# Performance work log

Hardware: AMD Instinct MI355X
Metric: run time of the kernel (lower is better)

The kernel has to match this reference:

```python
import jax, jax.numpy as jnp
import numpy as np

B, S, D, H, DK, DV, DFF = 16, 1024, 512, 8, 64, 64, 2048


def _layernorm(x, g, b, eps):
    mu = jnp.mean(x, axis=-1, keepdims=True)
    var = jnp.mean((x - mu) ** 2, axis=-1, keepdims=True)
    return (x - mu) / jnp.sqrt(var + eps) * g + b


def setup_inputs() -> dict:
    key = jax.random.key(0)
    ks = jax.random.split(key, 18)
    def lin_w(k, out_d, in_d):
        lim = np.sqrt(6.0 / (in_d + out_d))  # xavier_uniform
        return jax.random.uniform(k, (out_d, in_d), jnp.float32, -lim, lim)
    return {
        'x': jax.random.normal(ks[0], (B, S, D), jnp.float32),
        'wq': lin_w(ks[1], H * DK, D), 'bq': jnp.zeros((H * DK,), jnp.float32),
        'wk': lin_w(ks[2], H * DK, D), 'bk': jnp.zeros((H * DK,), jnp.float32),
        'wv': lin_w(ks[3], H * DV, D), 'bv': jnp.zeros((H * DV,), jnp.float32),
        'wfc': lin_w(ks[4], D, H * DV), 'bfc': jnp.zeros((D,), jnp.float32),
        'ln1_g': jnp.ones((D,), jnp.float32), 'ln1_b': jnp.zeros((D,), jnp.float32),
        'w1f': lin_w(ks[5], DFF, D), 'b1f': jnp.zeros((DFF,), jnp.float32),
        'w2f': lin_w(ks[6], D, DFF), 'b2f': jnp.zeros((D,), jnp.float32),
        'ln2_g': jnp.ones((D,), jnp.float32), 'ln2_b': jnp.zeros((D,), jnp.float32),
        'current': 1,
    }


def reference(x, wq, bq, wk, bk, wv, bv, wfc, bfc, ln1_g, ln1_b,
              w1f, b1f, w2f, b2f, ln2_g, ln2_b, current):
    b, s, d = x.shape
    # QKV projections -> (b, h, s, d_head)
    q = (x @ wq.T + bq).reshape(b, s, H, DK).transpose(0, 2, 1, 3)
    k = (x @ wk.T + bk).reshape(b, s, H, DK).transpose(0, 2, 1, 3)
    v = (x @ wv.T + bv).reshape(b, s, H, DV).transpose(0, 2, 1, 3)
    # causal mask with variable diagonal (tril(ones, diagonal=-current))
    mask = jnp.tril(jnp.ones((s, s), jnp.float32), k=-int(current))
    temperature = jnp.float32(DK) ** 0.5
    scores = jnp.einsum('bhqd,bhkd->bhqk', q / temperature, k)
    scores = jnp.where(mask == 0, jnp.float32(-1e32), scores)
    attn = jax.nn.softmax(scores, axis=-1)  # [b,h,s,s]
    if int(current) == 1:  # zero-pad first query row
        attn = attn.at[:, :, 0, :].set(0.0)
    attn = attn * mask  # post-softmax mask multiply
    out = jnp.einsum('bhqk,bhkd->bhqd', attn, v)
    out = out.transpose(0, 2, 1, 3).reshape(b, s, H * DV)
    out = out @ wfc.T + bfc + x  # fc + residual (dropout = identity in eval)
    out = _layernorm(out, ln1_g, ln1_b, 1e-5)
    # position-wise FFN
    h = jax.nn.relu(out @ w1f.T + b1f)
    y = h @ w2f.T + b2f + out
    y = _layernorm(y, ln2_g, ln2_b, 1e-6)
    return y
```

## Files before the change

kernel.cpp:

```cpp
#include <hip/hip_runtime.h>
#include <hip/hip_bf16.h>
#include <stdint.h>
#include <stddef.h>

#define NB 16
#define NS 1024
#define ND 512
#define NH 8
#define NDFF 2048
#define NTOK (NB * NS)
#define LDK 1024

typedef __bf16 bf16;
typedef __attribute__((ext_vector_type(2))) __bf16 bf16x2;
typedef __attribute__((ext_vector_type(4))) __bf16 bf16x4;
typedef __attribute__((ext_vector_type(8))) __bf16 bf16x8;
typedef __attribute__((ext_vector_type(4))) float f32x4;

__device__ __forceinline__ void async_copy16(const void* g, void* l) {
  __builtin_amdgcn_global_load_lds(
      (const __attribute__((address_space(1))) void*)g,
      (__attribute__((address_space(3))) void*)l,
      16, 0, 0);
}

__global__ __launch_bounds__(256) void cvt_all(
    const float* __restrict__ x, const float* __restrict__ wq,
    const float* __restrict__ wk, const float* __restrict__ wv,
    const float* __restrict__ wfc, const float* __restrict__ w1f,
    const float* __restrict__ w2f,
    bf16* __restrict__ xb, bf16* __restrict__ w3b,
    bf16* __restrict__ wfcb, bf16* __restrict__ w1fb, bf16* __restrict__ w2fb) {
  constexpr int C0 = 2097152, C1 = C0 + 65536, C2 = C1 + 65536, C3 = C2 + 65536,
                C4 = C3 + 65536, C5 = C4 + 262144;
  const int i = blockIdx.x * 256 + threadIdx.x;
  const float* s;
  bf16* d;
  int base;
  if (i < C0)      { s = x;   d = xb;            base = 0;  }
  else if (i < C1) { s = wq;  d = w3b;           base = C0; }
  else if (i < C2) { s = wk;  d = w3b + 262144;  base = C1; }
  else if (i < C3) { s = wv;  d = w3b + 524288;  base = C2; }
  else if (i < C4) { s = wfc; d = wfcb;          base = C3; }
  else if (i < C5) { s = w1f; d = w1fb;          base = C4; }
  else             { s = w2f; d = w2fb;          base = C5; }
  const int k = i - base;
  const float4 v = ((const float4*)s)[k];
  bf16x4 o = {(bf16)v.x, (bf16)v.y, (bf16)v.z, (bf16)v.w};
  ((bf16x4*)d)[k] = o;
}

__global__ __launch_bounds__(512) void concat3(const float* __restrict__ a,
                                               const float* __restrict__ b,
                                               const float* __restrict__ c,
                                               float* __restrict__ o) {
  const int t = threadIdx.x;
  o[t] = a[t];
  o[512 + t] = b[t];
  o[1024 + t] = c[t];
}

__device__ __forceinline__ int swz_src_col(int lane) {
  const int r = lane >> 2, c = lane & 3;
  return (c ^ ((r >> 1) & 3)) * 8;
}

template <bool RELU, bool QKV, bool RESB>
__global__ __launch_bounds__(512, 4) void gemm_bt(
    const bf16* __restrict__ A, const bf16* __restrict__ Bw,
    const float* __restrict__ bias, bf16* __restrict__ Cb,
    bf16* __restrict__ Cvt, const bf16* __restrict__ residb,
    int M, int N, int K) {
  __shared__ bf16 As[2][256 * 32];
  __shared__ bf16 Bs[2][128 * 32];
  const int tid = threadIdx.x;
  const int lane = tid & 63;
  const int wid = tid >> 6;

  const int nwg = gridDim.x * gridDim.y;
  int id = blockIdx.y * gridDim.x + blockIdx.x;
  id = (id & 7) * (nwg >> 3) + (id >> 3);
  const int tn = id % gridDim.x, tm = id / gridDim.x;

  const int wm = wid >> 1, wn = wid & 1;
  const int lr = lane & 15, hi2 = lane >> 4;
  const int lkA = ((hi2 ^ ((lr >> 1) & 3)) << 3);
  const int srow = lane >> 2, scol = swz_src_col(lane);

  f32x4 acc[4][4] = {};

  const bf16* Abase = A + (size_t)(tm * 256 + srow) * K + scol;
  const bf16* Bbase = Bw + (size_t)(tn * 128 + srow) * K + scol;
  const int kiters = K >> 5;

  auto stage = [&](int buf, int kb) {
#pragma unroll
    for (int t = 0; t < 3; ++t) {
      const int c = wid * 3 + t;
      if (c < 16) {
        async_copy16(Abase + (size_t)c * 16 * K + kb * 32, &As[buf][c * 512]);
      } else {
        const int s = c - 16;
        async_copy16(Bbase + (size_t)s * 16 * K + kb * 32, &Bs[buf][s * 512]);
      }
    }
  };

  stage(0, 0);

  int buf = 0;
  for (int kb = 0; kb < kiters; ++kb) {
    if (kb + 1 < kiters) {
      stage(buf ^ 1, kb + 1);
      asm volatile("s_waitcnt vmcnt(3)" ::: "memory");
    } else {
      asm volatile("s_waitcnt vmcnt(0)" ::: "memory");
    }
    __builtin_amdgcn_s_barrier();
    __builtin_amdgcn_sched_barrier(0);

    bf16x8 af[4], bfr[4];
#pragma unroll
    for (int i = 0; i < 4; ++i)
      af[i] = *(const bf16x8*)&As[buf][(wm * 64 + i * 16 + lr) * 32 + lkA];
#pragma unroll
    for (int j = 0; j < 4; ++j)
      bfr[j] = *(const bf16x8*)&Bs[buf][(wn * 64 + j * 16 + lr) * 32 + lkA];
#pragma unroll
    for (int i = 0; i < 4; ++i)
#pragma unroll
      for (int j = 0; j < 4; ++j)
        acc[i][j] = __builtin_amdgcn_mfma_f32_16x16x32_bf16(af[i], bfr[j], acc[i][j], 0, 0, 0);

    __builtin_amdgcn_s_barrier();
    __builtin_amdgcn_sched_barrier(0);
    buf ^= 1;
  }

#pragma unroll
  for (int i = 0; i < 4; ++i) {
    const int row0 = tm * 256 + wm * 64 + i * 16 + hi2 * 4;
#pragma unroll
    for (int j = 0; j < 4; ++j) {
      const int col = tn * 128 + wn * 64 + j * 16 + lr;
      const float bcol = bias[col];
      if (QKV && col >= 1024) {
        bf16x4 ov;
#pragma unroll
        for (int r = 0; r < 4; ++r) ov[r] = (bf16)(acc[i][j][r] + bcol);
        *(bf16x4*)&Cvt[(size_t)(col - 1024) * M + row0] = ov;
      } else if (RESB) {
#pragma unroll
        for (int r = 0; r < 4; ++r) {
          const size_t idx = (size_t)(row0 + r) * N + col;
          Cb[idx] = (bf16)(acc[i][j][r] + bcol + (float)residb[idx]);
        }
      } else {
        const int strideN = QKV ? 1024 : N;
#pragma unroll
        for (int r = 0; r < 4; ++r) {
          float c = acc[i][j][r] + bcol;
          if (RELU) c = fmaxf(c, 0.f);
          Cb[(size_t)(row0 + r) * strideN + col] = (bf16)c;
        }
      }
    }
  }
}

__global__ __launch_bounds__(512) void gemm_ln(
    const bf16* __restrict__ A, const bf16* __restrict__ Bw,
    const float* __restrict__ bias, const bf16* __restrict__ resid,
    bf16* __restrict__ outB,
    const float* __restrict__ gam, const float* __restrict__ bet,
    float eps, int K) {
  __shared__ bf16 As[2][64 * 32];
  __shared__ bf16 Bs[2][512 * 32];
  __shared__ float red[8 * 32 * 2];
  const int tid = threadIdx.x;
  const int lane = tid & 63;
  const int wid = tid >> 6;
  const int wm = wid >> 2, wn = wid & 3;
  const int lr = lane & 15, hi2 = lane >> 4;
  const int lkA = ((hi2 ^ ((lr >> 1) & 3)) << 3);
  const int tm = blockIdx.x;

  f32x4 acc[2][8] = {};
  const int kiters = K >> 5;
  const int r4 = lane >> 2, c4 = swz_src_col(lane);

  auto stage = [&](int buf, int kb) {
    if (wid < 4) {
      async_copy16(A + (size_t)(tm * 64 + wid * 16 + r4) * K + kb * 32 + c4,
                   &As[buf][wid * 16 * 32]);
#pragma unroll
      for (int i = 0; i < 3; ++i) {
        const int s = wid * 3 + i;
        async_copy16(Bw + (size_t)(s * 16 + r4) * K + kb * 32 + c4, &Bs[buf][s * 16 * 32]);
      }
    } else {
#pragma unroll
      for (int i = 0; i < 5; ++i) {
        const int s = 12 + (wid - 4) * 5 + i;
        async_copy16(Bw + (size_t)(s * 16 + r4) * K + kb * 32 + c4, &Bs[buf][s * 16 * 32]);
      }
    }
  };

  stage(0, 0);

  int buf = 0;
  for (int kb = 0; kb < kiters; ++kb) {
    if (kb + 1 < kiters) {
      stage(buf ^ 1, kb + 1);
      if (wid < 4) asm volatile("s_waitcnt vmcnt(4)" ::: "memory");
      else         asm volatile("s_waitcnt vmcnt(5)" ::: "memory");
    } else {
      asm volatile("s_waitcnt vmcnt(0)" ::: "memory");
    }
    __builtin_amdgcn_s_barrier();
    __builtin_amdgcn_sched_barrier(0);

    bf16x8 af[2], bfr[8];
#pragma unroll
    for (int i = 0; i < 2; ++i)
      af[i] = *(const bf16x8*)&As[buf][(wm * 32 + i * 16 + lr) * 32 + lkA];
#pragma unroll
    for (int j = 0; j < 8; ++j)
      bfr[j] = *(const bf16x8*)&Bs[buf][(wn * 128 + j * 16 + lr) * 32 + lkA];
#pragma unroll
    for (int i = 0; i < 2; ++i)
#pragma unroll
      for (int j = 0; j < 8; ++j)
        acc[i][j] = __builtin_amdgcn_mfma_f32_16x16x32_bf16(af[i], bfr[j], acc[i][j], 0, 0, 0);

    __builtin_amdgcn_s_barrier();
    __builtin_amdgcn_sched_barrier(0);
    buf ^= 1;
  }

  float bi[8];
#pragma unroll
  for (int j = 0; j < 8; ++j) bi[j] = bias[wn * 128 + j * 16 + lr];
#pragma unroll
  for (int i = 0; i < 2; ++i)
#pragma unroll
    for (int r = 0; r < 4; ++r) {
      const int rowg = tm * 64 + wm * 32 + i * 16 + hi2 * 4 + r;
#pragma unroll
      for (int j = 0; j < 8; ++j)
        acc[i][j][r] += bi[j] + (float)resid[(size_t)rowg * ND + wn * 128 + j * 16 + lr];
    }
#pragma unroll
  for (int i = 0; i < 2; ++i)
#pragma unroll
    for (int r = 0; r < 4; ++r) {
      float s = 0.f, s2 = 0.f;
#pragma unroll
      for (int j = 0; j < 8; ++j) {
        const float v = acc[i][j][r];
        s += v;
        s2 += v * v;
      }
#pragma unroll
      for (int o = 1; o < 16; o <<= 1) {
        s += __shfl_xor(s, o, 64);
        s2 += __shfl_xor(s2, o, 64);
      }
      if (lr == 0) {
        red[(wid * 32 + i * 16 + hi2 * 4 + r) * 2 + 0] = s;
        red[(wid * 32 + i * 16 + hi2 * 4 + r) * 2 + 1] = s2;
      }
    }
  __syncthreads();
  float g8[8], be8[8];
#pragma unroll
  for (int j = 0; j < 8; ++j) {
    g8[j] = gam[wn * 128 + j * 16 + lr];
    be8[j] = bet[wn * 128 + j * 16 + lr];
  }
#pragma unroll
  for (int i = 0; i < 2; ++i)
#pragma unroll
    for (int r = 0; r < 4; ++r) {
      const int rlw = i * 16 + hi2 * 4 + r;
      float S = 0.f, S2 = 0.f;
#pragma unroll
      for (int q = 0; q < 4; ++q) {
        S += red[((wm * 4 + q) * 32 + rlw) * 2 + 0];
        S2 += red[((wm * 4 + q) * 32 + rlw) * 2 + 1];
      }
      const float mu = S * (1.f / ND);
      const float rstd = rsqrtf(S2 * (1.f / ND) - mu * mu + eps);
      const int rowg = tm * 64 + wm * 32 + rlw;
#pragma unroll
      for (int j = 0; j < 8; ++j) {
        const float ln = (acc[i][j][r] - mu) * rstd * g8[j] + be8[j];
        outB[(size_t)rowg * ND + wn * 128 + j * 16 + lr] = (bf16)ln;
      }
    }
}

__global__ __launch_bounds__(256) void layernorm_b(
    const bf16* __restrict__ in, const float* __restrict__ gam,
    const float* __restrict__ bet, float eps, float* __restrict__ outf) {
  const int row = blockIdx.x * 4 + (threadIdx.x >> 6);
  const int lane = threadIdx.x & 63;
  const bf16x8 v = ((const bf16x8*)(in + (size_t)row * ND))[lane];
  float f[8];
  float s = 0.f, s2 = 0.f;
#pragma unroll
  for (int e = 0; e < 8; ++e) {
    f[e] = (float)v[e];
    s += f[e];
    s2 += f[e] * f[e];
  }
#pragma unroll
  for (int off = 1; off < 64; off <<= 1) {
    s += __shfl_xor(s, off, 64);
    s2 += __shfl_xor(s2, off, 64);
  }
  const float mu = s * (1.f / ND);
  const float var = s2 * (1.f / ND) - mu * mu;
  const float rstd = rsqrtf(var + eps);
  const float4 g0 = ((const float4*)gam)[lane * 2];
  const float4 g1 = ((const float4*)gam)[lane * 2 + 1];
  const float4 b0 = ((const float4*)bet)[lane * 2];
  const float4 b1 = ((const float4*)bet)[lane * 2 + 1];
  float4 o0, o1;
  o0.x = (f[0] - mu) * rstd * g0.x + b0.x;
  o0.y = (f[1] - mu) * rstd * g0.y + b0.y;
  o0.z = (f[2] - mu) * rstd * g0.z + b0.z;
  o0.w = (f[3] - mu) * rstd * g0.w + b0.w;
  o1.x = (f[4] - mu) * rstd * g1.x + b1.x;
  o1.y = (f[5] - mu) * rstd * g1.y + b1.y;
  o1.z = (f[6] - mu) * rstd * g1.z + b1.z;
  o1.w = (f[7] - mu) * rstd * g1.w + b1.w;
  float* op = outf + (size_t)row * ND;
  ((float4*)op)[lane * 2] = o0;
  ((float4*)op)[lane * 2 + 1] = o1;
}

__global__ __launch_bounds__(512) void attn_k(
    const bf16* __restrict__ QKg, const bf16* __restrict__ VTg,
    bf16* __restrict__ O, const int* __restrict__ curp) {
  const int current = *curp;
  const int bh = blockIdx.x;
  const int b = bh >> 3, h = bh & 7;
  const int q0 = (gridDim.y - 1 - blockIdx.y) * 128;
  const int tid = threadIdx.x, lane = tid & 63, wid = tid >> 6;
  const int lr = lane & 15, hi2 = lane >> 4, lk = hi2 * 8;

  __shared__ bf16 Kt[2][64 * 64];
  __shared__ bf16 Vt2[2][64 * 64];
  __shared__ bf16 Pw[8][16 * 76];

  const size_t qoff = (size_t)(b * NS + q0 + wid * 16 + lr) * LDK + h * 64 + lk;
  const bf16x8 aq0 = *(const bf16x8*)&QKg[qoff];
  const bf16x8 aq1 = *(const bf16x8*)&QKg[qoff + 32];

  f32x4 acc[4] = {};
  float m_run = -1e30f, l_run = 0.f;

  int kmax = q0 + 127 - current;
  if (kmax > NS - 1) kmax = NS - 1;
  const int nkt = (kmax >= 0) ? ((kmax >> 6) + 1) : 0;
  const float SCL2 = 0.18033688f;
  const int qv = q0 + wid * 16 + lr;

  const int kchunk = (lane & 7) ^ (lane >> 3);
  const int vdv = wid * 8 + (lane >> 3);
  const int vkeyc = ((lane & 7) ^ (lane >> 3)) * 8;

  auto stageKV = [&](int kt_, int buf_) {
    const int k0_ = kt_ * 64;
    const int rloc = wid * 8 + (lane >> 3);
    async_copy16(&QKg[(size_t)(b * NS + k0_ + rloc) * LDK + 512 + h * 64 + kchunk * 8],
                 &Kt[buf_][wid * 512]);
    async_copy16(&VTg[(size_t)(h * 64 + vdv) * NTOK + b * NS + k0_ + vkeyc],
                 &Vt2[buf_][wid * 512]);
  };

  if (nkt > 0) stageKV(0, 0);

  for (int kt = 0; kt < nkt; ++kt) {
    const int buf = kt & 1;
    if (kt + 1 < nkt) {
      stageKV(kt + 1, buf ^ 1);
      asm volatile("s_waitcnt vmcnt(2)" ::: "memory");
    } else {
      asm volatile("s_waitcnt vmcnt(0)" ::: "memory");
    }
    __builtin_amdgcn_s_barrier();
    __builtin_amdgcn_sched_barrier(0);

    const int k0 = kt * 64;
    const bf16* Ktb = &Kt[buf][0];
    const bf16* Vtb = &Vt2[buf][0];

    f32x4 sf[4];
    __builtin_amdgcn_s_setprio(1);
#pragma unroll
    for (int kc = 0; kc < 4; ++kc) {
      const int row = kc * 16 + lr;
      const int idx0 = row * 64 + ((hi2 ^ (lr & 7)) << 3);
      f32x4 z = {};
      const bf16x8 bk0 = *(const bf16x8*)&Ktb[idx0];
      const bf16x8 bk1 = *(const bf16x8*)&Ktb[idx0 ^ 32];
      z = __builtin_amdgcn_mfma_f32_16x16x32_bf16(bk0, aq0, z, 0, 0, 0);
      z = __builtin_amdgcn_mfma_f32_16x16x32_bf16(bk1, aq1, z, 0, 0, 0);
      sf[kc] = z;
    }
    __builtin_amdgcn_s_setprio(0);

    float sv[16];
    float mx = -1e30f;
    const bool full = (k0 + 63 + current <= q0 + wid * 16);
    if (full) {
#pragma unroll
      for (int kc = 0; kc < 4; ++kc)
#pragma unroll
        for (int r = 0; r < 4; ++r) {
          const float s = sf[kc][r] * SCL2;
          sv[kc * 4 + r] = s;
          mx = fmaxf(mx, s);
        }
    } else {
      const int keyb = k0 + hi2 * 4;
#pragma unroll
      for (int kc = 0; kc < 4; ++kc)
#pragma unroll
        for (int r = 0; r < 4; ++r) {
          const int key = keyb + kc * 16 + r;
          const float s = (key + current <= qv) ? sf[kc][r] * SCL2 : -3.0e38f;
          sv[kc * 4 + r] = s;
          mx = fmaxf(mx, s);
        }
    }
    mx = fmaxf(mx, __shfl_xor(mx, 16, 64));
    mx = fmaxf(mx, __shfl_xor(mx, 32, 64));
    if (__any(mx - m_run > 8.f)) {
      const float mnew = fmaxf(m_run, mx);
      const float sc = __builtin_amdgcn_exp2f(m_run - mnew);
      m_run = mnew;
      l_run *= sc;
#pragma unroll
      for (int j = 0; j < 4; ++j)
#pragma unroll
        for (int r = 0; r < 4; ++r) acc[j][r] *= sc;
    }
    float ps = 0.f;
    bf16x4 pb[4];
#pragma unroll
    for (int kc = 0; kc < 4; ++kc)
#pragma unroll
      for (int r = 0; r < 4; ++r) {
        const float p = __builtin_amdgcn_exp2f(sv[kc * 4 + r] - m_run);
        ps += p;
        pb[kc][r] = (bf16)p;
      }
    ps += __shfl_xor(ps, 16, 64);
    ps += __shfl_xor(ps, 32, 64);
    l_run += ps;
#pragma unroll
    for (int kc = 0; kc < 4; ++kc)
      *(bf16x4*)&Pw[wid][lr * 76 + kc * 16 + hi2 * 4] = pb[kc];

    __builtin_amdgcn_s_setprio(1);
#pragma unroll
    for (int kk = 0; kk < 2; ++kk) {
      const bf16x8 ap = *(const bf16x8*)&Pw[wid][lr * 76 + kk * 32 + lk];
      const int kbase = kk * 4 + hi2;
#pragma unroll
      for (int j = 0; j < 4; ++j) {
        const int dv = j * 16 + lr;
        const bf16x8 bv = *(const bf16x8*)&Vtb[dv * 64 + ((kbase ^ (dv & 7)) << 3)];
        acc[j] = __builtin_amdgcn_mfma_f32_16x16x32_bf16(bv, ap, acc[j], 0, 0, 0);
      }
    }
    __builtin_amdgcn_s_setprio(0);
    __builtin_amdgcn_s_barrier();
    __builtin_amdgcn_sched_barrier(0);
  }

  const float linv = (l_run > 0.f) ? 1.f / l_run : 0.f;
#pragma unroll
  for (int j = 0; j < 4; ++j) {
    bf16x4 ov;
#pragma unroll
    for (int r = 0; r < 4; ++r) ov[r] = (bf16)(acc[j][r] * linv);
    *(bf16x4*)&O[(size_t)(b * NS + qv) * ND + h * 64 + j * 16 + hi2 * 4] = ov;
  }
}

extern "C" void kernel_launch(void* const* d_in, const int* in_sizes, int n_in,
                              void* d_out, int out_size, void* d_ws, size_t ws_size,
                              hipStream_t stream) {
  const float* x = (const float*)d_in[0];
  const float* wq = (const float*)d_in[1];
  const float* bq = (const float*)d_in[2];
  const float* wk = (const float*)d_in[3];
  const float* bk = (const float*)d_in[4];
  const float* wv = (const float*)d_in[5];
  const float* bv = (const float*)d_in[6];
  const float* wfc = (const float*)d_in[7];
  const float* bfc = (const float*)d_in[8];
  const float* ln1g = (const float*)d_in[9];
  const float* ln1b = (const float*)d_in[10];
  const float* w1f = (const float*)d_in[11];
  const float* b1f = (const float*)d_in[12];
  const float* w2f = (const float*)d_in[13];
  const float* b2f = (const float*)d_in[14];
  const float* ln2g = (const float*)d_in[15];
  const float* ln2b = (const float*)d_in[16];
  const int* cur = (const int*)d_in[17];
  float* out = (float*)d_out;

  char* ws = (char*)d_ws;
  size_t off = 0;
  auto alloc = [&](size_t bytes) {
    void* p = ws + off;
    off += (bytes + 255) & ~(size_t)255;
    return p;
  };
  bf16* xb = (bf16*)alloc((size_t)NTOK * ND * 2);
  bf16* AO = (bf16*)alloc((size_t)NTOK * ND * 2);
  bf16* w3b = (bf16*)alloc((size_t)3 * ND * ND * 2);
  bf16* wfcb = (bf16*)alloc((size_t)ND * ND * 2);
  bf16* w1fb = (bf16*)alloc((size_t)NDFF * ND * 2);
  bf16* w2fb = (bf16*)alloc((size_t)ND * NDFF * 2);
  float* b3 = (float*)alloc((size_t)3 * ND * 4);
  bf16* qkb = (bf16*)alloc((size_t)NTOK * LDK * 2);
  bf16* VTg = (bf16*)alloc((size_t)ND * NTOK * 2);
  bf16* hb = (bf16*)alloc((size_t)NTOK * NDFF * 2);
  bf16* sum2 = (bf16*)alloc((size_t)NTOK * ND * 2);
  bf16* ln1bb = qkb;

  cvt_all<<<dim3(11264), dim3(256), 0, stream>>>(x, wq, wk, wv, wfc, w1f, w2f,
                                                 xb, w3b, wfcb, w1fb, w2fb);
  concat3<<<dim3(1), dim3(512), 0, stream>>>(bq, bk, bv, b3);

  gemm_bt<false, true, false><<<dim3(1536 / 128, NTOK / 256), dim3(512), 0, stream>>>(
      xb, w3b, b3, qkb, VTg, nullptr, NTOK, 1536, ND);
  attn_k<<<dim3(NB * NH, NS / 128), dim3(512), 0, stream>>>(qkb, VTg, AO, cur);
  gemm_ln<<<dim3(NTOK / 64), dim3(512), 0, stream>>>(
      AO, wfcb, bfc, xb, ln1bb, ln1g, ln1b, 1e-5f, ND);
  gemm_bt<true, false, false><<<dim3(NDFF / 128, NTOK / 256), dim3(512), 0, stream>>>(
      ln1bb, w1fb, b1f, hb, nullptr, nullptr, NTOK, NDFF, ND);
  gemm_bt<false, false, true><<<dim3(ND / 128, NTOK / 256), dim3(512), 0, stream>>>(
      hb, w2fb, b2f, sum2, nullptr, ln1bb, NTOK, ND, NDFF);
  layernorm_b<<<dim3(NTOK / 4), dim3(256), 0, stream>>>(sum2, ln2g, ln2b, 1e-6f, out);
}
```

Baseline: 211.0 us.

## Process two 128-query tiles per attention block to reuse staged K/V

Each attention block now covers 256 queries as two 128-row fragments, each warp holding two query fragments with separate online-softmax state and accumulators. Each staged K/V tile is therefore used twice, halving global K/V traffic and barrier overhead per query. The softmax scale is also folded into Q at load time, which adds bf16 rounding to the pre-scaled Q. The grid shrinks to half as many blocks, so parallelism, causal load balance and register pressure all change.

```diff
diff --git a/kernel.cpp b/kernel.cpp
--- a/kernel.cpp
+++ b/kernel.cpp
@@ -347,7 +347,7 @@
   const int current = *curp;
   const int bh = blockIdx.x;
   const int b = bh >> 3, h = bh & 7;
-  const int q0 = (gridDim.y - 1 - blockIdx.y) * 128;
+  const int q0 = (gridDim.y - 1 - blockIdx.y) * 256;
   const int tid = threadIdx.x, lane = tid & 63, wid = tid >> 6;
   const int lr = lane & 15, hi2 = lane >> 4, lk = hi2 * 8;
 
@@ -355,18 +355,28 @@
   __shared__ bf16 Vt2[2][64 * 64];
   __shared__ bf16 Pw[8][16 * 76];
 
-  const size_t qoff = (size_t)(b * NS + q0 + wid * 16 + lr) * LDK + h * 64 + lk;
-  const bf16x8 aq0 = *(const bf16x8*)&QKg[qoff];
-  const bf16x8 aq1 = *(const bf16x8*)&QKg[qoff + 32];
-
-  f32x4 acc[4] = {};
-  float m_run = -1e30f, l_run = 0.f;
-
-  int kmax = q0 + 127 - current;
+  const float SCL2 = 0.18033688f;
+
+  bf16x8 aq0[2], aq1[2];
+#pragma unroll
+  for (int f = 0; f < 2; ++f) {
+    const size_t qoff =
+        (size_t)(b * NS + q0 + f * 128 + wid * 16 + lr) * LDK + h * 64 + lk;
+    const bf16x8 r0 = *(const bf16x8*)&QKg[qoff];
+    const bf16x8 r1 = *(const bf16x8*)&QKg[qoff + 32];
+#pragma unroll
+    for (int e = 0; e < 8; ++e) {
+      aq0[f][e] = (bf16)((float)r0[e] * SCL2);
+      aq1[f][e] = (bf16)((float)r1[e] * SCL2);
+    }
+  }
+
+  f32x4 acc[2][4] = {};
+  float m_run[2] = {-1e30f, -1e30f}, l_run[2] = {0.f, 0.f};
+
+  int kmax = q0 + 255 - current;
   if (kmax > NS - 1) kmax = NS - 1;
   const int nkt = (kmax >= 0) ? ((kmax >> 6) + 1) : 0;
-  const float SCL2 = 0.18033688f;
-  const int qv = q0 + wid * 16 + lr;
 
   const int kchunk = (lane & 7) ^ (lane >> 3);
   const int vdv = wid * 8 + (lane >> 3);
@@ -398,98 +408,109 @@
     const bf16* Ktb = &Kt[buf][0];
     const bf16* Vtb = &Vt2[buf][0];
 
-    f32x4 sf[4];
-    __builtin_amdgcn_s_setprio(1);
-#pragma unroll
-    for (int kc = 0; kc < 4; ++kc) {
-      const int row = kc * 16 + lr;
-      const int idx0 = row * 64 + ((hi2 ^ (lr & 7)) << 3);
-      f32x4 z = {};
-      const bf16x8 bk0 = *(const bf16x8*)&Ktb[idx0];
-      const bf16x8 bk1 = *(const bf16x8*)&Ktb[idx0 ^ 32];
-      z = __builtin_amdgcn_mfma_f32_16x16x32_bf16(bk0, aq0, z, 0, 0, 0);
-      z = __builtin_amdgcn_mfma_f32_16x16x32_bf16(bk1, aq1, z, 0, 0, 0);
-      sf[kc] = z;
-    }
-    __builtin_amdgcn_s_setprio(0);
-
-    float sv[16];
-    float mx = -1e30f;
-    const bool full = (k0 + 63 + current <= q0 + wid * 16);
-    if (full) {
+#pragma unroll
+    for (int f = 0; f < 2; ++f) {
+      const int qbase = q0 + f * 128 + wid * 16;
+      if (k0 + current > qbase + 15) continue;
+      const int qv = qbase + lr;
+
+      f32x4 sf[4];
+      __builtin_amdgcn_s_setprio(1);
+#pragma unroll
+      for (int kc = 0; kc < 4; ++kc) {
+        const int row = kc * 16 + lr;
+        const int idx0 = row * 64 + ((hi2 ^ (lr & 7)) << 3);
+        f32x4 z = {};
+        const bf16x8 bk0 = *(const bf16x8*)&Ktb[idx0];
+        const bf16x8 bk1 = *(const bf16x8*)&Ktb[idx0 ^ 32];
+        z = __builtin_amdgcn_mfma_f32_16x16x32_bf16(bk0, aq0[f], z, 0, 0, 0);
+        z = __builtin_amdgcn_mfma_f32_16x16x32_bf16(bk1, aq1[f], z, 0, 0, 0);
+        sf[kc] = z;
+      }
+      __builtin_amdgcn_s_setprio(0);
+
+      float sv[16];
+      float mx = -1e30f;
+      const bool full = (k0 + 63 + current <= qbase);
+      if (full) {
+#pragma unroll
+        for (int kc = 0; kc < 4; ++kc)
+#pragma unroll
+          for (int r = 0; r < 4; ++r) {
+            const float s = sf[kc][r];
+            sv[kc * 4 + r] = s;
+            mx = fmaxf(mx, s);
+          }
+      } else {
+        const int keyb = k0 + hi2 * 4;
+#pragma unroll
+        for (int kc = 0; kc < 4; ++kc)
+#pragma unroll
+          for (int r = 0; r < 4; ++r) {
+            const int key = keyb + kc * 16 + r;
+            const float s = (key + current <= qv) ? sf[kc][r] : -3.0e38f;
+            sv[kc * 4 + r] = s;
+            mx = fmaxf(mx, s);
+          }
+      }
+      mx = fmaxf(mx, __shfl_xor(mx, 16, 64));
+      mx = fmaxf(mx, __shfl_xor(mx, 32, 64));
+      if (__any(mx - m_run[f] > 8.f)) {
+        const float mnew = fmaxf(m_run[f], mx);
+        const float sc = __builtin_amdgcn_exp2f(m_run[f] - mnew);
+        m_run[f] = mnew;
+        l_run[f] *= sc;
+#pragma unroll
+        for (int j = 0; j < 4; ++j)
+#pragma unroll
+          for (int r = 0; r < 4; ++r) acc[f][j][r] *= sc;
+      }
+      float ps = 0.f;
+      bf16x4 pb[4];
 #pragma unroll
       for (int kc = 0; kc < 4; ++kc)
 #pragma unroll
         for (int r = 0; r < 4; ++r) {
-          const float s = sf[kc][r] * SCL2;
-          sv[kc * 4 + r] = s;
-          mx = fmaxf(mx, s);
+          const float p = __builtin_amdgcn_exp2f(sv[kc * 4 + r] - m_run[f]);
+          ps += p;
+          pb[kc][r] = (bf16)p;
         }
-    } else {
-      const int keyb = k0 + hi2 * 4;
+      ps += __shfl_xor(ps, 16, 64);
+      ps += __shfl_xor(ps, 32, 64);
+      l_run[f] += ps;
 #pragma unroll
       for (int kc = 0; kc < 4; ++kc)
-#pragma unroll
-        for (int r = 0; r < 4; ++r) {
-          const int key = keyb + kc * 16 + r;
-          const float s = (key + current <= qv) ? sf[kc][r] * SCL2 : -3.0e38f;
-          sv[kc * 4 + r] = s;
-          mx = fmaxf(mx, s);
+        *(bf16x4*)&Pw[wid][lr * 76 + kc * 16 + hi2 * 4] = pb[kc];
+
+      __builtin_amdgcn_s_setprio(1);
+#pragma unroll
+      for (int kk = 0; kk < 2; ++kk) {
+        const bf16x8 ap = *(const bf16x8*)&Pw[wid][lr * 76 + kk * 32 + lk];
+        const int kbase = kk * 4 + hi2;
+#pragma unroll
+        for (int j = 0; j < 4; ++j) {
+          const int dv = j * 16 + lr;
+          const bf16x8 bv = *(const bf16x8*)&Vtb[dv * 64 + ((kbase ^ (dv & 7)) << 3)];
+          acc[f][j] = __builtin_amdgcn_mfma_f32_16x16x32_bf16(bv, ap, acc[f][j], 0, 0, 0);
         }
-    }
-    mx = fmaxf(mx, __shfl_xor(mx, 16, 64));
-    mx = fmaxf(mx, __shfl_xor(mx, 32, 64));
-    if (__any(mx - m_run > 8.f)) {
-      const float mnew = fmaxf(m_run, mx);
-      const float sc = __builtin_amdgcn_exp2f(m_run - mnew);
-      m_run = mnew;
-      l_run *= sc;
-#pragma unroll
-      for (int j = 0; j < 4; ++j)
-#pragma unroll
-        for (int r = 0; r < 4; ++r) acc[j][r] *= sc;
-    }
-    float ps = 0.f;
-    bf16x4 pb[4];
-#pragma unroll
-    for (int kc = 0; kc < 4; ++kc)
-#pragma unroll
-      for (int r = 0; r < 4; ++r) {
-        const float p = __builtin_amdgcn_exp2f(sv[kc * 4 + r] - m_run);
-        ps += p;
-        pb[kc][r] = (bf16)p;
-      }
-    ps += __shfl_xor(ps, 16, 64);
-    ps += __shfl_xor(ps, 32, 64);
-    l_run += ps;
-#pragma unroll
-    for (int kc = 0; kc < 4; ++kc)
-      *(bf16x4*)&Pw[wid][lr * 76 + kc * 16 + hi2 * 4] = pb[kc];
-
-    __builtin_amdgcn_s_setprio(1);
-#pragma unroll
-    for (int kk = 0; kk < 2; ++kk) {
-      const bf16x8 ap = *(const bf16x8*)&Pw[wid][lr * 76 + kk * 32 + lk];
-      const int kbase = kk * 4 + hi2;
-#pragma unroll
-      for (int j = 0; j < 4; ++j) {
-        const int dv = j * 16 + lr;
-        const bf16x8 bv = *(const bf16x8*)&Vtb[dv * 64 + ((kbase ^ (dv & 7)) << 3)];
-        acc[j] = __builtin_amdgcn_mfma_f32_16x16x32_bf16(bv, ap, acc[j], 0, 0, 0);
-      }
-    }
-    __builtin_amdgcn_s_setprio(0);
+      }
+      __builtin_amdgcn_s_setprio(0);
+    }
     __builtin_amdgcn_s_barrier();
     __builtin_amdgcn_sched_barrier(0);
   }
 
-  const float linv = (l_run > 0.f) ? 1.f / l_run : 0.f;
-#pragma unroll
-  for (int j = 0; j < 4; ++j) {
-    bf16x4 ov;
-#pragma unroll
-    for (int r = 0; r < 4; ++r) ov[r] = (bf16)(acc[j][r] * linv);
-    *(bf16x4*)&O[(size_t)(b * NS + qv) * ND + h * 64 + j * 16 + hi2 * 4] = ov;
+#pragma unroll
+  for (int f = 0; f < 2; ++f) {
+    const int qv = q0 + f * 128 + wid * 16 + lr;
+    const float linv = (l_run[f] > 0.f) ? 1.f / l_run[f] : 0.f;
+#pragma unroll
+    for (int j = 0; j < 4; ++j) {
+      bf16x4 ov;
+#pragma unroll
+      for (int r = 0; r < 4; ++r) ov[r] = (bf16)(acc[f][j][r] * linv);
+      *(bf16x4*)&O[(size_t)(b * NS + qv) * ND + h * 64 + j * 16 + hi2 * 4] = ov;
+    }
   }
 }
 
@@ -542,7 +563,7 @@
 
   gemm_bt<false, true, false><<<dim3(1536 / 128, NTOK / 256), dim3(512), 0, stream>>>(
       xb, w3b, b3, qkb, VTg, nullptr, NTOK, 1536, ND);
-  attn_k<<<dim3(NB * NH, NS / 128), dim3(512), 0, stream>>>(qkb, VTg, AO, cur);
+  attn_k<<<dim3(NB * NH, NS / 256), dim3(512), 0, stream>>>(qkb, VTg, AO, cur);
   gemm_ln<<<dim3(NTOK / 64), dim3(512), 0, stream>>>(
       AO, wfcb, bfc, xb, ln1bb, ln1g, ln1b, 1e-5f, ND);
   gemm_bt<true, false, false><<<dim3(NDFF / 128, NTOK / 256), dim3(512), 0, stream>>>(
```

New measurement: 212.4 us. About the same (+0.7%).
